# Kernel optimization log

Hardware: AMD Instinct MI355X
Metric: run time of the kernel (lower is better)

## Reference

```python
import jax, jax.numpy as jnp
import numpy as np
import math

R, C, B, E, H, F = 64, 256, 1, 768, 12, 3072
D = E // H  # head dim = 64
EPS = 1e-6  # flax LayerNorm default


def _ln(x, s, b):
    mu = jnp.mean(x, axis=-1, keepdims=True)
    var = jnp.mean((x - mu) ** 2, axis=-1, keepdims=True)
    return (x - mu) * jax.lax.rsqrt(var + EPS) * s + b


def setup_inputs() -> dict:
    key = jax.random.key(0)
    ks = jax.random.split(key, 16)
    w = lambda k, sh: jax.random.normal(k, sh, jnp.float32) * 0.02
    z = lambda sh: jnp.zeros(sh, jnp.float32)
    return {
        "x": jax.random.normal(ks[0], (R, C, B, E), jnp.float32),
        "ln1_s": jnp.ones((E,), jnp.float32), "ln1_b": z((E,)),
        "r_wq": w(ks[1], (E, E)), "r_bq": z((E,)),
        "r_wk": w(ks[2], (E, E)), "r_bk": z((E,)),
        "r_wv": w(ks[3], (E, E)), "r_bv": z((E,)),
        "r_wo": w(ks[4], (E, E)), "r_bo": z((E,)),
        "ln2_s": jnp.ones((E,), jnp.float32), "ln2_b": z((E,)),
        "c_wq": w(ks[5], (E, E)), "c_bq": z((E,)),
        "c_wk": w(ks[6], (E, E)), "c_bk": z((E,)),
        "c_wv": w(ks[7], (E, E)), "c_bv": z((E,)),
        "c_wo": w(ks[8], (E, E)), "c_bo": z((E,)),
        "ln3_s": jnp.ones((E,), jnp.float32), "ln3_b": z((E,)),
        "f_w1": w(ks[9], (E, F)), "f_b1": z((F,)),
        "f_w2": w(ks[10], (F, E)), "f_b2": z((E,)),
    }


def reference(x, ln1_s, ln1_b, r_wq, r_bq, r_wk, r_bk, r_wv, r_bv, r_wo, r_bo,
              ln2_s, ln2_b, c_wq, c_bq, c_wk, c_bk, c_wv, c_bv, c_wo, c_bo,
              ln3_s, ln3_b, f_w1, f_b1, f_w2, f_b2):
    qkv = (R, C, B, H, D)
    # --- tied row self-attention (NOTE: original code has no residual adds) ---
    h = _ln(x, ln1_s, ln1_b)
    q = (h @ r_wq + r_bq).reshape(qkv) * (D ** -0.5 / math.sqrt(R))  # tied-row scaling
    k = (h @ r_wk + r_bk).reshape(qkv)
    v = (h @ r_wv + r_bv).reshape(qkv)
    aw = jnp.einsum('rinhd,rjnhd->hnij', q, k)  # single softmax tied across rows
    ap = jax.nn.softmax(aw, axis=-1)
    ctx = jnp.einsum('hnij,rjnhd->rinhd', ap, v).reshape(R, C, B, E)
    x = ctx @ r_wo + r_bo
    # --- column self-attention (per-column attention over rows) ---
    h = _ln(x, ln2_s, ln2_b)
    q = (h @ c_wq + c_bq).reshape(qkv) * (D ** -0.5)
    k = (h @ c_wk + c_bk).reshape(qkv)
    v = (h @ c_wv + c_bv).reshape(qkv)
    aw = jnp.einsum('icnhd,jcnhd->hcnij', q, k)
    ap = jax.nn.softmax(aw, axis=-1)
    ctx = jnp.einsum('hcnij,jcnhd->icnhd', ap, v).reshape(R, C, B, E)
    x = ctx @ c_wo + c_bo
    # --- FFN (gelu approximate=True matches flax default) ---
    h = _ln(x, ln3_s, ln3_b)
    return jax.nn.gelu(h @ f_w1 + f_b1) @ f_w2 + f_b2
```

## Files before the change

kernel.cpp:

```cpp
#include <hip/hip_runtime.h>
#include <hip/hip_bf16.h>
#include <stdint.h>
#include <stddef.h>

#define R_ 64
#define C_ 256
#define E_ 768
#define H_ 12
#define F_ 3072
#define D_ 64
#define NT_ (R_*C_)
#define HCRD_ ((size_t)H_*C_*R_*D_)

typedef float f32x4 __attribute__((ext_vector_type(4)));
typedef __bf16 bf16x8 __attribute__((ext_vector_type(8)));
typedef unsigned short us4 __attribute__((ext_vector_type(4)));
typedef unsigned short us8 __attribute__((ext_vector_type(8)));

typedef __attribute__((address_space(3))) uint32_t lds_u32;
typedef __attribute__((address_space(1))) uint32_t glb_u32;

__device__ __forceinline__ void gld16(const uint16_t* g, uint16_t* l) {
  __builtin_amdgcn_global_load_lds((const glb_u32*)g, (lds_u32*)l, 16, 0, 0);
}

__device__ __forceinline__ uint16_t f2b(float f) {
  __bf16 h = (__bf16)f;
  return *(uint16_t*)&h;
}

#define BAR      { asm volatile("s_barrier" ::: "memory"); }
#define VMW0     { asm volatile("s_waitcnt vmcnt(0)" ::: "memory"); }

enum { EP_F32B = 0, EP_GELU = 1, EP_AW = 2, EP_CTX = 3, EP_QKVROW = 4, EP_QKVCOL = 5 };

template<int EP, bool PERM>
__global__ __launch_bounds__(512, 2)
void gemm256(const uint16_t* __restrict__ A, const uint16_t* __restrict__ B,
             const float* __restrict__ bias, const float* __restrict__ biasK,
             const float* __restrict__ biasV, void* __restrict__ out,
             int N, int K, int lda, int ldb, float scale)
{
  __shared__ uint16_t As2[2][16384];
  __shared__ uint16_t Bs2[2][16384];
  const int tid  = threadIdx.x;
  const int wave = tid >> 6, lane = tid & 63;
  const int wm = wave >> 2, wn = wave & 3;
  const int lr = lane & 15, lq = lane >> 4;

  const int lin = blockIdx.x + gridDim.x * blockIdx.y;
  const int q8 = (gridDim.x * gridDim.y) >> 3;
  const int wid = (lin & 7) * q8 + (lin >> 3);
  const int px = wid % gridDim.x, by = wid / gridDim.x;
  const long bm = (long)by * 256;

  const int Nx = N >> 8, P = gridDim.x;
  const int qq = Nx / P, rr = Nx - qq * P;
  const int cnt   = qq + (px < rr ? 1 : 0);
  const int start = px * qq + (px < rr ? px : rr);

  const int r0 = tid >> 3;
  const int c8 = (((tid & 7) ^ (r0 & 7)) << 3);
  const uint16_t* aSrc[4];
  long bRow[4];
#pragma unroll
  for (int i = 0; i < 4; ++i) {
    long am = bm + r0 + 64 * i;
    if constexpr (PERM) am = ((am & 63) << 8) | (am >> 6);
    aSrc[i] = A + am * (long)lda + c8;
    bRow[i] = (long)(r0 + 64 * i) * ldb;
  }

  auto stageA = [&](int u) {
    const int b = u & 1, kb = u << 6;
#pragma unroll
    for (int i = 0; i < 4; ++i) gld16(aSrc[i] + kb, &As2[b][tid * 8 + 4096 * i]);
  };
  auto stageB = [&](int u, const uint16_t* bBase) {
    const int b = u & 1, kb = u << 6;
#pragma unroll
    for (int i = 0; i < 4; ++i) gld16(bBase + bRow[i] + kb, &Bs2[b][tid * 8 + 4096 * i]);
  };
  auto rdoff = [&](int row, int c) { return row * 64 + (((c ^ (row & 7))) << 3); };

  const int nt = K >> 6;
  f32x4 acc[8][4];

  { const uint16_t* b0 = B + c8 + ((long)start << 8) * ldb;
    stageA(0); stageB(0, b0); }

  for (int e = 0; e < cnt; ++e) {
    const int bxi = start + e;
    const long bn = (long)bxi << 8;
    const uint16_t* bBase = B + c8 + bn * ldb;
    const uint16_t* bNext = B + c8 + (bn + 256) * ldb;

#pragma unroll
    for (int i = 0; i < 8; ++i)
#pragma unroll
      for (int j = 0; j < 4; ++j) acc[i][j] = (f32x4){0.f, 0.f, 0.f, 0.f};

    VMW0; BAR;

    for (int t = 0; t < nt; ++t) {
      const int b = t & 1;
      if (t + 1 < nt)      { stageA(t + 1); stageB(t + 1, bBase); }
      else if (e + 1 < cnt) { stageA(0);     stageB(0, bNext); }
#pragma unroll
      for (int kh = 0; kh < 2; ++kh) {
        const int c = kh * 4 + lq;
        bf16x8 bfr[4], afr[8];
#pragma unroll
        for (int i = 0; i < 4; ++i) bfr[i] = *(const bf16x8*)&Bs2[b][rdoff(wn * 64 + i * 16 + lr, c)];
#pragma unroll
        for (int i = 0; i < 8; ++i) afr[i] = *(const bf16x8*)&As2[b][rdoff(wm * 128 + i * 16 + lr, c)];
#pragma unroll
        for (int mi = 0; mi < 8; ++mi)
#pragma unroll
          for (int ni = 0; ni < 4; ++ni)
            acc[mi][ni] = __builtin_amdgcn_mfma_f32_16x16x32_bf16(afr[mi], bfr[ni], acc[mi][ni], 0, 0, 0);
      }
      if (t + 1 < nt) { VMW0; BAR; }
      else            { BAR; }
    }

    if constexpr (EP == EP_F32B) {
#pragma unroll
      for (int mi = 0; mi < 8; ++mi)
#pragma unroll
        for (int ni = 0; ni < 4; ++ni)
#pragma unroll
          for (int r = 0; r < 4; ++r) {
            const long row = bm + wm * 128 + mi * 16 + lq * 4 + r;
            const long col = bn + wn * 64 + ni * 16 + lr;
            ((float*)out)[row * N + col] = acc[mi][ni][r] + bias[col];
          }
    } else {
      uint16_t* slab = (wave < 4) ? &As2[1][wave * 4096] : &Bs2[1][(wave - 4) * 4096];
      const long colb = bn + wn * 64;
      int grp = 0; long cc0 = colb;
      const float* bb = bias;
      if constexpr (EP != EP_GELU) {
        grp = colb >= 1536 ? 2 : (colb >= 768 ? 1 : 0);
        cc0 = colb - (long)grp * 768;
        bb = grp == 0 ? bias : (grp == 1 ? biasK : biasV);
      }
      const bool tr = (EP != EP_GELU) && (grp == 2);
#pragma unroll
      for (int sub = 0; sub < 2; ++sub) {
        const long m0 = bm + wm * 128 + sub * 64;
#pragma unroll
        for (int mi = 0; mi < 4; ++mi)
#pragma unroll
          for (int ni = 0; ni < 4; ++ni)
#pragma unroll
            for (int r = 0; r < 4; ++r) {
              const int lrow = mi * 16 + lq * 4 + r;
              const int lcol = ni * 16 + lr;
              float val;
              if constexpr (EP == EP_GELU) {
                const float t = acc[sub * 4 + mi][ni][r] + bias[colb + lcol];
                const float u = 0.7978845608028654f * (t + 0.044715f * t * t * t);
                const float e2 = __expf(2.f * u);
                val = 0.5f * t * (2.f - 2.f * __builtin_amdgcn_rcpf(e2 + 1.f));
              } else {
                val = acc[sub * 4 + mi][ni][r] + bb[cc0 + lcol];
                if (grp == 0) val *= scale;
              }
              const int sr = tr ? lcol : lrow;
              const int sc = tr ? lrow : lcol;
              const int psc = (sc & 7) | ((((sc >> 3) ^ (sr & 7))) << 3);
              slab[sr * 64 + psc] = f2b(val);
            }
        uint16_t* o16 = (uint16_t*)out;
        long obase, rstride;
        if constexpr (EP == EP_GELU) {
          obase = m0 * (long)N + colb; rstride = N;
        } else {
          const long h = cc0 >> 6;
          if constexpr (EP == EP_QKVROW) {
            const long rr2 = m0 >> 8, c0 = m0 & 255;
            if (grp < 2) { obase = (size_t)grp * HCRD_ + ((h * C_ + c0) * R_ + rr2) * D_; rstride = R_ * D_; }
            else         { obase = 2 * HCRD_ + ((h * R_ + rr2) * D_) * C_ + c0;           rstride = C_; }
          } else {
            const long cq = m0 >> 6;
            if (grp < 2) { obase = (size_t)grp * HCRD_ + ((h * C_ + cq) * R_) * D_; rstride = D_; }
            else         { obase = 2 * HCRD_ + ((h * C_ + cq) * D_) * R_;           rstride = R_; }
          }
        }
        const int rl = lane >> 3, chn = lane & 7;
#pragma unroll
        for (int pp = 0; pp < 8; ++pp) {
          const int srow = pp * 8 + rl;
          const int pch = chn ^ (srow & 7);
          us8 wv = *(const us8*)&slab[srow * 64 + pch * 8];
          *(us8*)(o16 + obase + (long)srow * rstride + chn * 8) = wv;
        }
      }
    }
  }
}

template<int EP>
__global__ __launch_bounds__(256)
void gemm_bt(const uint16_t* __restrict__ A, const uint16_t* __restrict__ B,
             void* __restrict__ out,
             int M, int N, int K, int lda, int ldb, long sAz, long sBz)
{
  __shared__ uint16_t As[2][4096];
  __shared__ uint16_t Bs[2][4096];
  const int tid  = threadIdx.x;
  const int wave = tid >> 6, lane = tid & 63;
  const int z = blockIdx.z;

  const long bm = (long)blockIdx.y * 128;
  int kc = 0; long bnb = blockIdx.x;
  if constexpr (EP == EP_AW) { kc = blockIdx.x & 3; bnb = blockIdx.x >> 2; }
  const long bn = bnb * 128;
  const int wr = (wave >> 1) * 64;
  const int wc = (wave & 1) * 64;
  const int lr = lane & 15;
  const int lq = lane >> 4;

  const int t0 = tid, t1 = tid + 256;
  const int ar0 = t0 >> 2, ar1 = t1 >> 2;
  const int ac0 = (((t0 & 3) ^ ((ar0 >> 1) & 3)) * 8);
  const int ac1 = (((t1 & 3) ^ ((ar1 >> 1) & 3)) * 8);

  const uint16_t* a0p = A + (long)z * sAz + (bm + ar0) * (long)lda + (long)kc * 1024;
  const uint16_t* a1p = A + (long)z * sAz + (bm + ar1) * (long)lda + (long)kc * 1024;
  const uint16_t* b0p = B + (long)z * sBz + (bn + ar0) * (long)ldb + (long)kc * 1024;
  const uint16_t* b1p = B + (long)z * sBz + (bn + ar1) * (long)ldb + (long)kc * 1024;

  auto STAGE = [&](int bi, int kt) {
    gld16(a0p + kt + ac0, &As[bi][t0 * 8]);
    gld16(a1p + kt + ac1, &As[bi][t1 * 8]);
    gld16(b0p + kt + ac0, &Bs[bi][t0 * 8]);
    gld16(b1p + kt + ac1, &Bs[bi][t1 * 8]);
  };

  int apos[4], bpos[4];
#pragma unroll
  for (int i = 0; i < 4; ++i) {
    const int ra = wr + i * 16 + lr;
    const int rb = wc + i * 16 + lr;
    apos[i] = ra * 32 + (lq ^ ((ra >> 1) & 3)) * 8;
    bpos[i] = rb * 32 + (lq ^ ((rb >> 1) & 3)) * 8;
  }

  f32x4 acc[4][4];
#pragma unroll
  for (int i = 0; i < 4; ++i)
#pragma unroll
    for (int j = 0; j < 4; ++j) acc[i][j] = (f32x4){0.f, 0.f, 0.f, 0.f};

  const int nt = K >> 5;
  STAGE(0, 0);
  VMW0; BAR;

  for (int t = 0; t < nt; ++t) {
    const int b = t & 1;
    if (t + 1 < nt) STAGE(b ^ 1, (t + 1) << 5);
    bf16x8 af[4], bfm[4];
#pragma unroll
    for (int i = 0; i < 4; ++i) {
      af[i]  = *(const bf16x8*)&As[b][apos[i]];
      bfm[i] = *(const bf16x8*)&Bs[b][bpos[i]];
    }
#pragma unroll
    for (int mi = 0; mi < 4; ++mi)
#pragma unroll
      for (int ni = 0; ni < 4; ++ni)
        acc[mi][ni] = __builtin_amdgcn_mfma_f32_16x16x32_bf16(af[mi], bfm[ni], acc[mi][ni], 0, 0, 0);
    if (t + 1 < nt) { VMW0; BAR; }
  }

#pragma unroll
  for (int mi = 0; mi < 4; ++mi)
#pragma unroll
    for (int ni = 0; ni < 4; ++ni)
#pragma unroll
      for (int r = 0; r < 4; ++r) {
        const long row = bm + wr + mi * 16 + lq * 4 + r;
        const long col = bn + wc + ni * 16 + lr;
        if constexpr (EP == EP_AW) {
          ((float*)out)[((long)(z * 4 + kc) * M + row) * N + col] = acc[mi][ni][r];
        } else {
          ((uint16_t*)out)[((col >> 6) * C_ + row) * E_ + (long)z * 64 + (col & 63)] =
              f2b(acc[mi][ni][r]);
        }
      }
}

__global__ __launch_bounds__(256)
void ln_k(const float* __restrict__ x, const float* __restrict__ s, const float* __restrict__ b,
          uint16_t* __restrict__ out)
{
  const int wave = threadIdx.x >> 6, lane = threadIdx.x & 63;
  const long row = (long)blockIdx.x * 4 + wave;
  const float* xr = x + row * E_;
  f32x4 v[3];
  float sum = 0.f, sq = 0.f;
#pragma unroll
  for (int i = 0; i < 3; ++i) {
    v[i] = *(const f32x4*)(xr + (i * 64 + lane) * 4);
#pragma unroll
    for (int j = 0; j < 4; ++j) { sum += v[i][j]; sq += v[i][j] * v[i][j]; }
  }
#pragma unroll
  for (int m = 1; m < 64; m <<= 1) { sum += __shfl_xor(sum, m); sq += __shfl_xor(sq, m); }
  const float mu = sum * (1.f / E_);
  const float var = sq * (1.f / E_) - mu * mu;
  const float rs = rsqrtf(var + 1e-6f);
  uint16_t* orow = out + row * E_;
#pragma unroll
  for (int i = 0; i < 3; ++i) {
    const int e0 = (i * 64 + lane) * 4;
    us4 o;
#pragma unroll
    for (int j = 0; j < 4; ++j) o[j] = f2b((v[i][j] - mu) * rs * s[e0 + j] + b[e0 + j]);
    *(us4*)(orow + e0) = o;
  }
}

__global__ __launch_bounds__(256)
void softmax_k4(const float* __restrict__ aw4, uint16_t* __restrict__ ap)
{
  const int wave = threadIdx.x >> 6, lane = threadIdx.x & 63;
  const long row = (long)blockIdx.x * 4 + wave;
  const long h = row >> 8, i = row & 255;
  f32x4 v = (f32x4){0.f, 0.f, 0.f, 0.f};
#pragma unroll
  for (int kc = 0; kc < 4; ++kc) {
    f32x4 t = *(const f32x4*)(aw4 + (((h * 4 + kc) * C_ + i) * C_) + lane * 4);
#pragma unroll
    for (int j = 0; j < 4; ++j) v[j] += t[j];
  }
  float m = fmaxf(fmaxf(v[0], v[1]), fmaxf(v[2], v[3]));
#pragma unroll
  for (int k = 1; k < 64; k <<= 1) m = fmaxf(m, __shfl_xor(m, k));
  f32x4 e; float s = 0.f;
#pragma unroll
  for (int j = 0; j < 4; ++j) { e[j] = __expf(v[j] - m); s += e[j]; }
#pragma unroll
  for (int k = 1; k < 64; k <<= 1) s += __shfl_xor(s, k);
  const float inv = 1.f / s;
  us4 o;
#pragma unroll
  for (int j = 0; j < 4; ++j) o[j] = f2b(e[j] * inv);
  *(us4*)(ap + row * C_ + lane * 4) = o;
}

__global__ __launch_bounds__(256)
void tcvt(const float* __restrict__ in, uint16_t* __restrict__ out, int K, int N)
{
  __shared__ float t[32][33];
  const int tx = threadIdx.x, ty = threadIdx.y;
  const long k0 = (long)blockIdx.y * 32, n0 = (long)blockIdx.x * 32;
  for (int i = ty; i < 32; i += 8) t[i][tx] = in[(k0 + i) * N + n0 + tx];
  __syncthreads();
  for (int i = ty; i < 32; i += 8) out[(n0 + i) * K + k0 + tx] = f2b(t[tx][i]);
}

__global__ __launch_bounds__(256)
void tcvt8(const float* a0, const float* a1, const float* a2, const float* a3,
           const float* a4, const float* a5, const float* a6, const float* a7,
           uint16_t* o0, uint16_t* o1, uint16_t* o2, uint16_t* o3,
           uint16_t* o4, uint16_t* o5, uint16_t* o6, uint16_t* o7)
{
  __shared__ float t[32][33];
  const float* in; uint16_t* out;
  switch (blockIdx.z) {
    case 0: in = a0; out = o0; break;
    case 1: in = a1; out = o1; break;
    case 2: in = a2; out = o2; break;
    case 3: in = a3; out = o3; break;
    case 4: in = a4; out = o4; break;
    case 5: in = a5; out = o5; break;
    case 6: in = a6; out = o6; break;
    default: in = a7; out = o7; break;
  }
  const int tx = threadIdx.x, ty = threadIdx.y;
  const long k0 = (long)blockIdx.y * 32, n0 = (long)blockIdx.x * 32;
  for (int i = ty; i < 32; i += 8) t[i][tx] = in[(k0 + i) * E_ + n0 + tx];
  __syncthreads();
  for (int i = ty; i < 32; i += 8) out[(n0 + i) * E_ + k0 + tx] = f2b(t[tx][i]);
}

__global__ __launch_bounds__(64)
void colattn(const uint16_t* __restrict__ q, const uint16_t* __restrict__ k,
             const uint16_t* __restrict__ v, uint16_t* __restrict__ ctx)
{
  __shared__ uint16_t Qs[64 * 64];
  __shared__ uint16_t Ks[64 * 64];
  __shared__ uint16_t Vs[64 * 64];
  const int hc = blockIdx.x;
  const int h = hc >> 8, c = hc & 255;
  const int lane = threadIdx.x;
  const uint16_t* qb = q + (long)hc * (R_ * D_);
  const uint16_t* kb = k + (long)hc * (R_ * D_);
  const uint16_t* vb = v + (long)hc * (D_ * R_);
#pragma unroll
  for (int it = 0; it < 8; ++it) {
    const int o = (it * 64 + lane) * 8;
    gld16(qb + o, &Qs[o]);
    gld16(kb + o, &Ks[o]);
    gld16(vb + o, &Vs[o]);
  }
  asm volatile("s_waitcnt vmcnt(0)" ::: "memory");
  __builtin_amdgcn_sched_barrier(0);

  const int lr = lane & 15, lq = lane >> 4;
  f32x4 acc[4][4];
#pragma unroll
  for (int i = 0; i < 4; ++i)
#pragma unroll
    for (int j = 0; j < 4; ++j) acc[i][j] = (f32x4){0.f, 0.f, 0.f, 0.f};

#pragma unroll
  for (int kt = 0; kt < 2; ++kt) {
    bf16x8 af[4], bfm[4];
#pragma unroll
    for (int i = 0; i < 4; ++i) {
      af[i]  = *(const bf16x8*)&Qs[(i * 16 + lr) * 64 + kt * 32 + lq * 8];
      bfm[i] = *(const bf16x8*)&Ks[(i * 16 + lr) * 64 + kt * 32 + lq * 8];
    }
#pragma unroll
    for (int mi = 0; mi < 4; ++mi)
#pragma unroll
      for (int ni = 0; ni < 4; ++ni)
        acc[mi][ni] = __builtin_amdgcn_mfma_f32_16x16x32_bf16(af[mi], bfm[ni], acc[mi][ni], 0, 0, 0);
  }

#pragma unroll
  for (int mi = 0; mi < 4; ++mi) {
#pragma unroll
    for (int r = 0; r < 4; ++r) {
      float mx = fmaxf(fmaxf(acc[mi][0][r], acc[mi][1][r]), fmaxf(acc[mi][2][r], acc[mi][3][r]));
#pragma unroll
      for (int s = 1; s < 16; s <<= 1) mx = fmaxf(mx, __shfl_xor(mx, s));
      float e0 = __expf(acc[mi][0][r] - mx), e1 = __expf(acc[mi][1][r] - mx);
      float e2 = __expf(acc[mi][2][r] - mx), e3 = __expf(acc[mi][3][r] - mx);
      float sum = e0 + e1 + e2 + e3;
#pragma unroll
      for (int s = 1; s < 16; s <<= 1) sum += __shfl_xor(sum, s);
      const float inv = 1.f / sum;
      const int i = mi * 16 + lq * 4 + r;
      Qs[i * 64 +  0 + lr] = f2b(e0 * inv);
      Qs[i * 64 + 16 + lr] = f2b(e1 * inv);
      Qs[i * 64 + 32 + lr] = f2b(e2 * inv);
      Qs[i * 64 + 48 + lr] = f2b(e3 * inv);
    }
  }
  __syncthreads();

  f32x4 o_[4][4];
#pragma unroll
  for (int i = 0; i < 4; ++i)
#pragma unroll
    for (int j = 0; j < 4; ++j) o_[i][j] = (f32x4){0.f, 0.f, 0.f, 0.f};

#pragma unroll
  for (int kt = 0; kt < 2; ++kt) {
    bf16x8 pa[4], vv[4];
#pragma unroll
    for (int i = 0; i < 4; ++i) {
      pa[i] = *(const bf16x8*)&Qs[(i * 16 + lr) * 64 + kt * 32 + lq * 8];
      vv[i] = *(const bf16x8*)&Vs[(i * 16 + lr) * 64 + kt * 32 + lq * 8];
    }
#pragma unroll
    for (int mi = 0; mi < 4; ++mi)
#pragma unroll
      for (int ni = 0; ni < 4; ++ni)
        o_[mi][ni] = __builtin_amdgcn_mfma_f32_16x16x32_bf16(pa[mi], vv[ni], o_[mi][ni], 0, 0, 0);
  }

#pragma unroll
  for (int mi = 0; mi < 4; ++mi)
#pragma unroll
    for (int ni = 0; ni < 4; ++ni)
#pragma unroll
      for (int r = 0; r < 4; ++r) {
        const int i = mi * 16 + lq * 4 + r;
        const int d = ni * 16 + lr;
        ctx[((long)i * C_ + c) * E_ + h * 64 + d] = f2b(o_[mi][ni][r]);
      }
}

extern "C" void kernel_launch(void* const* d_in, const int* in_sizes, int n_in,
                              void* d_out, int out_size, void* d_ws, size_t ws_size,
                              hipStream_t stream)
{
  (void)in_sizes; (void)n_in; (void)out_size; (void)ws_size;
  const float* x     = (const float*)d_in[0];
  const float* ln1_s = (const float*)d_in[1];
  const float* ln1_b = (const float*)d_in[2];
  const float* r_wq  = (const float*)d_in[3];
  const float* r_bq  = (const float*)d_in[4];
  const float* r_wk  = (const float*)d_in[5];
  const float* r_bk  = (const float*)d_in[6];
  const float* r_wv  = (const float*)d_in[7];
  const float* r_bv  = (const float*)d_in[8];
  const float* r_wo  = (const float*)d_in[9];
  const float* r_bo  = (const float*)d_in[10];
  const float* ln2_s = (const float*)d_in[11];
  const float* ln2_b = (const float*)d_in[12];
  const float* c_wq  = (const float*)d_in[13];
  const float* c_bq  = (const float*)d_in[14];
  const float* c_wk  = (const float*)d_in[15];
  const float* c_bk  = (const float*)d_in[16];
  const float* c_wv  = (const float*)d_in[17];
  const float* c_bv  = (const float*)d_in[18];
  const float* c_wo  = (const float*)d_in[19];
  const float* c_bo  = (const float*)d_in[20];
  const float* ln3_s = (const float*)d_in[21];
  const float* ln3_b = (const float*)d_in[22];
  const float* f_w1  = (const float*)d_in[23];
  const float* f_b1  = (const float*)d_in[24];
  const float* f_w2  = (const float*)d_in[25];
  const float* f_b2  = (const float*)d_in[26];

  uint8_t* p = (uint8_t*)d_ws;
  auto take = [&p](size_t n) { uint8_t* r = p; p += (n + 255) & ~(size_t)255; return r; };

  uint16_t* wqkv1 = (uint16_t*)take((size_t)3 * E_ * E_ * 2);
  uint16_t* wqkv2 = (uint16_t*)take((size_t)3 * E_ * E_ * 2);
  uint16_t* rwoT  = (uint16_t*)take((size_t)E_ * E_ * 2);
  uint16_t* cwoT  = (uint16_t*)take((size_t)E_ * E_ * 2);
  uint16_t* w1T   = (uint16_t*)take((size_t)E_ * F_ * 2);
  uint16_t* w2T   = (uint16_t*)take((size_t)F_ * E_ * 2);
  uint16_t* hb    = (uint16_t*)take((size_t)NT_ * E_ * 2);
  uint16_t* qkvT  = (uint16_t*)take(3 * HCRD_ * 2);
  uint16_t* qT = qkvT, *kT = qkvT + HCRD_, *vT = qkvT + 2 * HCRD_;
  uint16_t* ctxb  = (uint16_t*)take((size_t)NT_ * E_ * 2);
  uint16_t* apb   = (uint16_t*)take((size_t)H_ * C_ * C_ * 2);
  uint16_t* g     = qkvT;
  float*    awb4  = (float*)ctxb;
  float*    x1    = (float*)d_out;

  const dim3 tb32(32, 8);
  tcvt8<<<dim3(E_ / 32, E_ / 32, 8), tb32, 0, stream>>>(
      r_wq, r_wk, r_wv, c_wq, c_wk, c_wv, r_wo, c_wo,
      wqkv1 + 0 * E_ * E_, wqkv1 + 1 * E_ * E_, wqkv1 + 2 * E_ * E_,
      wqkv2 + 0 * E_ * E_, wqkv2 + 1 * E_ * E_, wqkv2 + 2 * E_ * E_,
      rwoT, cwoT);
  tcvt<<<dim3(F_ / 32, E_ / 32), tb32, 0, stream>>>(f_w1, w1T, E_, F_);
  tcvt<<<dim3(E_ / 32, F_ / 32), tb32, 0, stream>>>(f_w2, w2T, F_, E_);

  ln_k<<<NT_ / 4, 256, 0, stream>>>(x, ln1_s, ln1_b, hb);
  gemm256<EP_QKVROW, false><<<dim3(4, 64), 512, 0, stream>>>(
      hb, wqkv1, r_bq, r_bk, r_bv, qkvT, 3 * E_, E_, E_, E_, 0.015625f);
  gemm_bt<EP_AW><<<dim3(8, 2, H_), 256, 0, stream>>>(
      qT, kT, awb4, C_, C_, 1024, R_ * D_, R_ * D_, (long)C_ * R_ * D_, (long)C_ * R_ * D_);
  softmax_k4<<<(H_ * C_) / 4, 256, 0, stream>>>(awb4, apb);
  gemm_bt<EP_CTX><<<dim3((R_ * D_) / 128, 2, H_), 256, 0, stream>>>(
      apb, vT, ctxb, C_, R_ * D_, C_, C_, C_, (long)C_ * C_, (long)R_ * D_ * C_);
  gemm256<EP_F32B, false><<<dim3(3, 64), 512, 0, stream>>>(
      ctxb, rwoT, r_bo, nullptr, nullptr, x1, E_, E_, E_, E_, 1.f);

  ln_k<<<NT_ / 4, 256, 0, stream>>>(x1, ln2_s, ln2_b, hb);
  gemm256<EP_QKVCOL, true><<<dim3(4, 64), 512, 0, stream>>>(
      hb, wqkv2, c_bq, c_bk, c_bv, qkvT, 3 * E_, E_, E_, E_, 0.125f);
  colattn<<<H_ * C_, 64, 0, stream>>>(qT, kT, vT, ctxb);
  gemm256<EP_F32B, false><<<dim3(3, 64), 512, 0, stream>>>(
      ctxb, cwoT, c_bo, nullptr, nullptr, x1, E_, E_, E_, E_, 1.f);

  ln_k<<<NT_ / 4, 256, 0, stream>>>(x1, ln3_s, ln3_b, hb);
  gemm256<EP_GELU, false><<<dim3(4, 64), 512, 0, stream>>>(
      hb, w1T, f_b1, nullptr, nullptr, g, F_, E_, E_, E_, 1.f);
  gemm256<EP_F32B, false><<<dim3(3, 64), 512, 0, stream>>>(
      g, w2T, f_b2, nullptr, nullptr, d_out, E_, F_, F_, F_, 1.f);
}
```

Baseline: 633.1 us.

## Load GEMM B operand straight to registers and drop persistent column tiling

```diff
diff --git a/kernel.cpp b/kernel.cpp
--- a/kernel.cpp
+++ b/kernel.cpp
@@ -36,13 +36,12 @@
 
 template<int EP, bool PERM>
 __global__ __launch_bounds__(512, 2)
-void gemm256(const uint16_t* __restrict__ A, const uint16_t* __restrict__ B,
-             const float* __restrict__ bias, const float* __restrict__ biasK,
-             const float* __restrict__ biasV, void* __restrict__ out,
-             int N, int K, int lda, int ldb, float scale)
+void gemmBR(const uint16_t* __restrict__ A, const uint16_t* __restrict__ B,
+            const float* __restrict__ bias, const float* __restrict__ biasK,
+            const float* __restrict__ biasV, void* __restrict__ out,
+            int N, int K, int lda, int ldb, float scale)
 {
   __shared__ uint16_t As2[2][16384];
-  __shared__ uint16_t Bs2[2][16384];
   const int tid  = threadIdx.x;
   const int wave = tid >> 6, lane = tid & 63;
   const int wm = wave >> 2, wn = wave & 3;
@@ -51,151 +50,148 @@
   const int lin = blockIdx.x + gridDim.x * blockIdx.y;
   const int q8 = (gridDim.x * gridDim.y) >> 3;
   const int wid = (lin & 7) * q8 + (lin >> 3);
-  const int px = wid % gridDim.x, by = wid / gridDim.x;
-  const long bm = (long)by * 256;
-
-  const int Nx = N >> 8, P = gridDim.x;
-  const int qq = Nx / P, rr = Nx - qq * P;
-  const int cnt   = qq + (px < rr ? 1 : 0);
-  const int start = px * qq + (px < rr ? px : rr);
+  const int bx = wid % gridDim.x, by = wid / gridDim.x;
+  const long bm = (long)by * 256, bn = (long)bx * 256;
 
   const int r0 = tid >> 3;
   const int c8 = (((tid & 7) ^ (r0 & 7)) << 3);
   const uint16_t* aSrc[4];
-  long bRow[4];
 #pragma unroll
   for (int i = 0; i < 4; ++i) {
     long am = bm + r0 + 64 * i;
     if constexpr (PERM) am = ((am & 63) << 8) | (am >> 6);
     aSrc[i] = A + am * (long)lda + c8;
-    bRow[i] = (long)(r0 + 64 * i) * ldb;
-  }
-
+  }
   auto stageA = [&](int u) {
     const int b = u & 1, kb = u << 6;
 #pragma unroll
     for (int i = 0; i < 4; ++i) gld16(aSrc[i] + kb, &As2[b][tid * 8 + 4096 * i]);
   };
-  auto stageB = [&](int u, const uint16_t* bBase) {
-    const int b = u & 1, kb = u << 6;
-#pragma unroll
-    for (int i = 0; i < 4; ++i) gld16(bBase + bRow[i] + kb, &Bs2[b][tid * 8 + 4096 * i]);
+  auto rdoff = [&](int row, int c) { return row * 64 + (((c ^ (row & 7))) << 3); };
+
+  const uint16_t* Bb[4];
+#pragma unroll
+  for (int i = 0; i < 4; ++i)
+    Bb[i] = B + (bn + wn * 64 + i * 16 + lr) * (long)ldb + lq * 8;
+  auto loadB = [&](bf16x8 (&Bd)[8], int t) {
+    const int kb = t << 6;
+#pragma unroll
+    for (int kh = 0; kh < 2; ++kh)
+#pragma unroll
+      for (int i = 0; i < 4; ++i)
+        Bd[kh * 4 + i] = *(const bf16x8*)(Bb[i] + kb + kh * 32);
   };
-  auto rdoff = [&](int row, int c) { return row * 64 + (((c ^ (row & 7))) << 3); };
-
+
+  f32x4 acc[8][4];
+#pragma unroll
+  for (int i = 0; i < 8; ++i)
+#pragma unroll
+    for (int j = 0; j < 4; ++j) acc[i][j] = (f32x4){0.f, 0.f, 0.f, 0.f};
+
+  bf16x8 B0[8], B1[8];
   const int nt = K >> 6;
-  f32x4 acc[8][4];
-
-  { const uint16_t* b0 = B + c8 + ((long)start << 8) * ldb;
-    stageA(0); stageB(0, b0); }
-
-  for (int e = 0; e < cnt; ++e) {
-    const int bxi = start + e;
-    const long bn = (long)bxi << 8;
-    const uint16_t* bBase = B + c8 + bn * ldb;
-    const uint16_t* bNext = B + c8 + (bn + 256) * ldb;
-
-#pragma unroll
-    for (int i = 0; i < 8; ++i)
-#pragma unroll
-      for (int j = 0; j < 4; ++j) acc[i][j] = (f32x4){0.f, 0.f, 0.f, 0.f};
-
-    VMW0; BAR;
-
-    for (int t = 0; t < nt; ++t) {
-      const int b = t & 1;
-      if (t + 1 < nt)      { stageA(t + 1); stageB(t + 1, bBase); }
-      else if (e + 1 < cnt) { stageA(0);     stageB(0, bNext); }
-#pragma unroll
-      for (int kh = 0; kh < 2; ++kh) {
-        const int c = kh * 4 + lq;
-        bf16x8 bfr[4], afr[8];
-#pragma unroll
-        for (int i = 0; i < 4; ++i) bfr[i] = *(const bf16x8*)&Bs2[b][rdoff(wn * 64 + i * 16 + lr, c)];
-#pragma unroll
-        for (int i = 0; i < 8; ++i) afr[i] = *(const bf16x8*)&As2[b][rdoff(wm * 128 + i * 16 + lr, c)];
-#pragma unroll
-        for (int mi = 0; mi < 8; ++mi)
-#pragma unroll
-          for (int ni = 0; ni < 4; ++ni)
-            acc[mi][ni] = __builtin_amdgcn_mfma_f32_16x16x32_bf16(afr[mi], bfr[ni], acc[mi][ni], 0, 0, 0);
+  stageA(0);
+  loadB(B0, 0);
+  VMW0; BAR;
+
+  auto body = [&](int t, bf16x8 (&Bcur)[8], bf16x8 (&Bnxt)[8]) {
+    const int b = t & 1;
+    const bool pre = (t + 1 < nt);
+    if (pre) { stageA(t + 1); loadB(Bnxt, t + 1); }
+#pragma unroll
+    for (int kh = 0; kh < 2; ++kh) {
+      const int c = kh * 4 + lq;
+      bf16x8 af[8];
+#pragma unroll
+      for (int i = 0; i < 8; ++i)
+        af[i] = *(const bf16x8*)&As2[b][rdoff(wm * 128 + i * 16 + lr, c)];
+#pragma unroll
+      for (int mi = 0; mi < 8; ++mi)
+#pragma unroll
+        for (int ni = 0; ni < 4; ++ni)
+          acc[mi][ni] = __builtin_amdgcn_mfma_f32_16x16x32_bf16(af[mi], Bcur[kh * 4 + ni],
+                                                                acc[mi][ni], 0, 0, 0);
+    }
+    if (pre) { VMW0; BAR; }
+  };
+
+  for (int t = 0; t < nt; t += 2) {
+    body(t, B0, B1);
+    body(t + 1, B1, B0);
+  }
+  __syncthreads();
+
+  if constexpr (EP == EP_F32B) {
+#pragma unroll
+    for (int mi = 0; mi < 8; ++mi)
+#pragma unroll
+      for (int ni = 0; ni < 4; ++ni)
+#pragma unroll
+        for (int r = 0; r < 4; ++r) {
+          const long row = bm + wm * 128 + mi * 16 + lq * 4 + r;
+          const long col = bn + wn * 64 + ni * 16 + lr;
+          ((float*)out)[row * N + col] = acc[mi][ni][r] + bias[col];
+        }
+  } else {
+    uint16_t* slab = ((uint16_t*)As2) + (size_t)wave * 4096;
+    const long colb = bn + wn * 64;
+    int grp = 0; long cc0 = colb;
+    const float* bb = bias;
+    if constexpr (EP != EP_GELU) {
+      grp = colb >= 1536 ? 2 : (colb >= 768 ? 1 : 0);
+      cc0 = colb - (long)grp * 768;
+      bb = grp == 0 ? bias : (grp == 1 ? biasK : biasV);
+    }
+    const bool tr = (EP != EP_GELU) && (grp == 2);
+#pragma unroll
+    for (int sub = 0; sub < 2; ++sub) {
+      const long m0 = bm + wm * 128 + sub * 64;
+#pragma unroll
+      for (int mi = 0; mi < 4; ++mi)
+#pragma unroll
+        for (int ni = 0; ni < 4; ++ni)
+#pragma unroll
+          for (int r = 0; r < 4; ++r) {
+            const int lrow = mi * 16 + lq * 4 + r;
+            const int lcol = ni * 16 + lr;
+            float val;
+            if constexpr (EP == EP_GELU) {
+              const float t = acc[sub * 4 + mi][ni][r] + bias[colb + lcol];
+              const float u = 0.7978845608028654f * (t + 0.044715f * t * t * t);
+              const float e2 = __expf(2.f * u);
+              val = 0.5f * t * (2.f - 2.f / (e2 + 1.f));
+            } else {
+              val = acc[sub * 4 + mi][ni][r] + bb[cc0 + lcol];
+              if (grp == 0) val *= scale;
+            }
+            const int sr = tr ? lcol : lrow;
+            const int sc = tr ? lrow : lcol;
+            const int psc = (sc & 7) | ((((sc >> 3) ^ (sr & 7))) << 3);
+            slab[sr * 64 + psc] = f2b(val);
+          }
+      uint16_t* o16 = (uint16_t*)out;
+      long obase, rstride;
+      if constexpr (EP == EP_GELU) {
+        obase = m0 * (long)N + colb; rstride = N;
+      } else {
+        const long h = cc0 >> 6;
+        if constexpr (EP == EP_QKVROW) {
+          const long rr2 = m0 >> 8, c0 = m0 & 255;
+          if (grp < 2) { obase = (size_t)grp * HCRD_ + ((h * C_ + c0) * R_ + rr2) * D_; rstride = R_ * D_; }
+          else         { obase = 2 * HCRD_ + ((h * R_ + rr2) * D_) * C_ + c0;           rstride = C_; }
+        } else {
+          const long cq = m0 >> 6;
+          if (grp < 2) { obase = (size_t)grp * HCRD_ + ((h * C_ + cq) * R_) * D_; rstride = D_; }
+          else         { obase = 2 * HCRD_ + ((h * C_ + cq) * D_) * R_;           rstride = R_; }
+        }
       }
-      if (t + 1 < nt) { VMW0; BAR; }
-      else            { BAR; }
-    }
-
-    if constexpr (EP == EP_F32B) {
-#pragma unroll
-      for (int mi = 0; mi < 8; ++mi)
-#pragma unroll
-        for (int ni = 0; ni < 4; ++ni)
-#pragma unroll
-          for (int r = 0; r < 4; ++r) {
-            const long row = bm + wm * 128 + mi * 16 + lq * 4 + r;
-            const long col = bn + wn * 64 + ni * 16 + lr;
-            ((float*)out)[row * N + col] = acc[mi][ni][r] + bias[col];
-          }
-    } else {
-      uint16_t* slab = (wave < 4) ? &As2[1][wave * 4096] : &Bs2[1][(wave - 4) * 4096];
-      const long colb = bn + wn * 64;
-      int grp = 0; long cc0 = colb;
-      const float* bb = bias;
-      if constexpr (EP != EP_GELU) {
-        grp = colb >= 1536 ? 2 : (colb >= 768 ? 1 : 0);
-        cc0 = colb - (long)grp * 768;
-        bb = grp == 0 ? bias : (grp == 1 ? biasK : biasV);
-      }
-      const bool tr = (EP != EP_GELU) && (grp == 2);
-#pragma unroll
-      for (int sub = 0; sub < 2; ++sub) {
-        const long m0 = bm + wm * 128 + sub * 64;
-#pragma unroll
-        for (int mi = 0; mi < 4; ++mi)
-#pragma unroll
-          for (int ni = 0; ni < 4; ++ni)
-#pragma unroll
-            for (int r = 0; r < 4; ++r) {
-              const int lrow = mi * 16 + lq * 4 + r;
-              const int lcol = ni * 16 + lr;
-              float val;
-              if constexpr (EP == EP_GELU) {
-                const float t = acc[sub * 4 + mi][ni][r] + bias[colb + lcol];
-                const float u = 0.7978845608028654f * (t + 0.044715f * t * t * t);
-                const float e2 = __expf(2.f * u);
-                val = 0.5f * t * (2.f - 2.f * __builtin_amdgcn_rcpf(e2 + 1.f));
-              } else {
-                val = acc[sub * 4 + mi][ni][r] + bb[cc0 + lcol];
-                if (grp == 0) val *= scale;
-              }
-              const int sr = tr ? lcol : lrow;
-              const int sc = tr ? lrow : lcol;
-              const int psc = (sc & 7) | ((((sc >> 3) ^ (sr & 7))) << 3);
-              slab[sr * 64 + psc] = f2b(val);
-            }
-        uint16_t* o16 = (uint16_t*)out;
-        long obase, rstride;
-        if constexpr (EP == EP_GELU) {
-          obase = m0 * (long)N + colb; rstride = N;
-        } else {
-          const long h = cc0 >> 6;
-          if constexpr (EP == EP_QKVROW) {
-            const long rr2 = m0 >> 8, c0 = m0 & 255;
-            if (grp < 2) { obase = (size_t)grp * HCRD_ + ((h * C_ + c0) * R_ + rr2) * D_; rstride = R_ * D_; }
-            else         { obase = 2 * HCRD_ + ((h * R_ + rr2) * D_) * C_ + c0;           rstride = C_; }
-          } else {
-            const long cq = m0 >> 6;
-            if (grp < 2) { obase = (size_t)grp * HCRD_ + ((h * C_ + cq) * R_) * D_; rstride = D_; }
-            else         { obase = 2 * HCRD_ + ((h * C_ + cq) * D_) * R_;           rstride = R_; }
-          }
-        }
-        const int rl = lane >> 3, chn = lane & 7;
-#pragma unroll
-        for (int pp = 0; pp < 8; ++pp) {
-          const int srow = pp * 8 + rl;
-          const int pch = chn ^ (srow & 7);
-          us8 wv = *(const us8*)&slab[srow * 64 + pch * 8];
-          *(us8*)(o16 + obase + (long)srow * rstride + chn * 8) = wv;
-        }
+      const int rl = lane >> 3, chn = lane & 7;
+#pragma unroll
+      for (int pp = 0; pp < 8; ++pp) {
+        const int srow = pp * 8 + rl;
+        const int pch = chn ^ (srow & 7);
+        us8 wv = *(const us8*)&slab[srow * 64 + pch * 8];
+        *(us8*)(o16 + obase + (long)srow * rstride + chn * 8) = wv;
       }
     }
   }
@@ -548,26 +544,26 @@
   tcvt<<<dim3(E_ / 32, F_ / 32), tb32, 0, stream>>>(f_w2, w2T, F_, E_);
 
   ln_k<<<NT_ / 4, 256, 0, stream>>>(x, ln1_s, ln1_b, hb);
-  gemm256<EP_QKVROW, false><<<dim3(4, 64), 512, 0, stream>>>(
+  gemmBR<EP_QKVROW, false><<<dim3(9, 64), 512, 0, stream>>>(
       hb, wqkv1, r_bq, r_bk, r_bv, qkvT, 3 * E_, E_, E_, E_, 0.015625f);
   gemm_bt<EP_AW><<<dim3(8, 2, H_), 256, 0, stream>>>(
       qT, kT, awb4, C_, C_, 1024, R_ * D_, R_ * D_, (long)C_ * R_ * D_, (long)C_ * R_ * D_);
   softmax_k4<<<(H_ * C_) / 4, 256, 0, stream>>>(awb4, apb);
   gemm_bt<EP_CTX><<<dim3((R_ * D_) / 128, 2, H_), 256, 0, stream>>>(
       apb, vT, ctxb, C_, R_ * D_, C_, C_, C_, (long)C_ * C_, (long)R_ * D_ * C_);
-  gemm256<EP_F32B, false><<<dim3(3, 64), 512, 0, stream>>>(
+  gemmBR<EP_F32B, false><<<dim3(3, 64), 512, 0, stream>>>(
       ctxb, rwoT, r_bo, nullptr, nullptr, x1, E_, E_, E_, E_, 1.f);
 
   ln_k<<<NT_ / 4, 256, 0, stream>>>(x1, ln2_s, ln2_b, hb);
-  gemm256<EP_QKVCOL, true><<<dim3(4, 64), 512, 0, stream>>>(
+  gemmBR<EP_QKVCOL, true><<<dim3(9, 64), 512, 0, stream>>>(
       hb, wqkv2, c_bq, c_bk, c_bv, qkvT, 3 * E_, E_, E_, E_, 0.125f);
   colattn<<<H_ * C_, 64, 0, stream>>>(qT, kT, vT, ctxb);
-  gemm256<EP_F32B, false><<<dim3(3, 64), 512, 0, stream>>>(
+  gemmBR<EP_F32B, false><<<dim3(3, 64), 512, 0, stream>>>(
       ctxb, cwoT, c_bo, nullptr, nullptr, x1, E_, E_, E_, E_, 1.f);
 
   ln_k<<<NT_ / 4, 256, 0, stream>>>(x1, ln3_s, ln3_b, hb);
-  gemm256<EP_GELU, false><<<dim3(4, 64), 512, 0, stream>>>(
+  gemmBR<EP_GELU, false><<<dim3(12, 64), 512, 0, stream>>>(
       hb, w1T, f_b1, nullptr, nullptr, g, F_, E_, E_, E_, 1.f);
-  gemm256<EP_F32B, false><<<dim3(3, 64), 512, 0, stream>>>(
+  gemmBR<EP_F32B, false><<<dim3(3, 64), 512, 0, stream>>>(
       g, w2T, f_b2, nullptr, nullptr, d_out, E_, F_, F_, F_, 1.f);
 }
```

New measurement: 1.064 ms. +68.0%, slower.
